# Kernel tuning notes

Measured on AMD Instinct MI355X. Metric: run time of the kernel, lower is better.

Reference implementation:

```python
import jax, jax.numpy as jnp
import numpy as np

NUM_HEADS = 16


def _rotate_half(x):
    x1, x2 = jnp.split(x, 2, axis=-1)
    return jnp.concatenate((-x2, x1), axis=-1)


def setup_inputs() -> dict:
    key = jax.random.key(0)
    ks = jax.random.split(key, 6)
    S, HID, D, W = 32768, 1280, 80, 64
    x = jax.random.normal(ks[0], (S, HID), dtype=jnp.float32)
    # rotary embeddings: use actual cos/sin of random phases for realism
    ang = jax.random.uniform(ks[1], (S, D), dtype=jnp.float32) * 6.28318
    cos = jnp.cos(ang)
    sin = jnp.sin(ang)
    # uniform windows of 64 tokens -> 512 windows
    cu_seqlens = (jnp.arange(S // W + 1, dtype=jnp.int32) * W)
    qkv_kernel = jax.random.normal(ks[2], (HID, 3 * HID), dtype=jnp.float32) * (HID ** -0.5)
    qkv_bias = jnp.zeros((3 * HID,), dtype=jnp.float32)
    proj_kernel = jax.random.normal(ks[3], (HID, HID), dtype=jnp.float32) * (HID ** -0.5)
    proj_bias = jnp.zeros((HID,), dtype=jnp.float32)
    return {"x": x, "cos": cos, "sin": sin, "cu_seqlens": cu_seqlens,
            "qkv_kernel": qkv_kernel, "qkv_bias": qkv_bias,
            "proj_kernel": proj_kernel, "proj_bias": proj_bias}


def reference(x, cos, sin, cu_seqlens, qkv_kernel, qkv_bias, proj_kernel, proj_bias):
    S, HID = x.shape
    H = NUM_HEADS
    D = HID // H
    scale = D ** -0.5

    qkv = x @ qkv_kernel + qkv_bias                      # [S, 3*HID]
    q, k, v = jnp.split(qkv, 3, axis=-1)
    q = q.reshape(S, H, D)
    k = k.reshape(S, H, D)
    v = v.reshape(S, H, D)

    c = cos[:, :D][:, None, :]                           # [S, 1, D]
    s = sin[:, :D][:, None, :]
    q = q * c + _rotate_half(q) * s
    k = k * c + _rotate_half(k) * s

    # Uniform windows: cu_seqlens = W * arange(nw+1); vectorize the per-window
    # full attention as a batched block-diagonal attention [nw, W, H, D].
    nw = cu_seqlens.shape[0] - 1
    W = S // nw
    qw = q.reshape(nw, W, H, D).astype(jnp.float32)
    kw = k.reshape(nw, W, H, D).astype(jnp.float32)
    vw = v.reshape(nw, W, H, D).astype(jnp.float32)

    scores = jnp.einsum('nqhd,nkhd->nhqk', qw, kw) * scale   # [nw, H, W, W]
    weights = jax.nn.softmax(scores, axis=-1)
    out = jnp.einsum('nhqk,nkhd->nqhd', weights, vw)          # [nw, W, H, D]
    out = out.reshape(S, HID).astype(x.dtype)
    return out @ proj_kernel + proj_bias
```

## Files before the change

kernel.cpp:

```cpp
#include <hip/hip_runtime.h>
#include <hip/hip_bf16.h>
#include <hip/hip_fp16.h>

typedef __attribute__((ext_vector_type(8))) short short8;
typedef __attribute__((ext_vector_type(4))) float f32x4;
typedef __attribute__((ext_vector_type(16))) float f32x16;
typedef unsigned short u16;
typedef unsigned int u32;

__device__ __forceinline__ u16 f2bf(float v) {
  __hip_bfloat16 h = __float2bfloat16(v);
  return __builtin_bit_cast(u16, h);
}
__device__ __forceinline__ float bf2f(u16 u) {
  return __builtin_bit_cast(float, (u32)u << 16);
}
__device__ __forceinline__ u16 f2h(float v) {
  __half h = __float2half(v);
  return __builtin_bit_cast(u16, h);
}
__device__ __forceinline__ float h2f(u16 u) {
  return __half2float(__builtin_bit_cast(__half, u));
}

__global__ __launch_bounds__(256) void casth(const float* __restrict__ X, long long n,
                                             u16* __restrict__ H) {
  long long i0 = ((long long)blockIdx.x * 256 + threadIdx.x) * 4;
  long long stride = (long long)gridDim.x * 256 * 4;
  for (long long i = i0; i < n; i += stride) {
    float4 v = *(const float4*)(X + i);
    ushort4 h;
    h.x = f2h(v.x);
    h.y = f2h(v.y);
    h.z = f2h(v.z);
    h.w = f2h(v.w);
    *(ushort4*)(H + i) = h;
  }
}

__global__ __launch_bounds__(256) void transpose_cast(const float* __restrict__ W,
    int K, int N, u16* __restrict__ T) {
  __shared__ float tile[64][65];
  const int nb = N >> 6;
  const int br = blockIdx.x / nb, bc = blockIdx.x - br * nb;
  const int tx = threadIdx.x & 63, ty = threadIdx.x >> 6;
  #pragma unroll
  for (int i = ty; i < 64; i += 4)
    tile[i][tx] = W[(size_t)(br * 64 + i) * N + bc * 64 + tx];
  __syncthreads();
  #pragma unroll
  for (int i = ty; i < 64; i += 4) {
    size_t off = (size_t)(bc * 64 + i) * K + br * 64 + tx;
    T[off] = f2h(tile[tx][i]);
  }
}

__global__ __launch_bounds__(256) void transpose_split(const float* __restrict__ W,
    int K, int N, u16* __restrict__ Thi, u16* __restrict__ Tlo) {
  __shared__ float tile[64][65];
  const int nb = N >> 6;
  const int br = blockIdx.x / nb, bc = blockIdx.x - br * nb;
  const int tx = threadIdx.x & 63, ty = threadIdx.x >> 6;
  #pragma unroll
  for (int i = ty; i < 64; i += 4)
    tile[i][tx] = W[(size_t)(br * 64 + i) * N + bc * 64 + tx];
  __syncthreads();
  #pragma unroll
  for (int i = ty; i < 64; i += 4) {
    float v = tile[tx][i];
    u16 hb = f2bf(v);
    size_t off = (size_t)(bc * 64 + i) * K + br * 64 + tx;
    Thi[off] = hb;
    Tlo[off] = f2bf(v - bf2f(hb));
  }
}

__global__ __launch_bounds__(256) void rope_qk(u16* __restrict__ qkv,
    const float* __restrict__ cosg, const float* __restrict__ sing) {
  const int idx = blockIdx.x * 256 + threadIdx.x;
  const int row = idx / 80;
  const int rem = idx - row * 80;
  const int h = rem / 5;
  const int dd = (rem - h * 5) * 8;
  u16* qp = qkv + (size_t)row * 3840 + h * 80 + dd;
  u16* kp = qp + 1280;
  const float* cp = cosg + row * 80 + dd;
  const float* sp = sing + row * 80 + dd;
  short8 qa = *(short8*)qp,        qb = *(short8*)(qp + 40);
  short8 ka = *(short8*)kp,        kb = *(short8*)(kp + 40);
  f32x4 cL0 = *(const f32x4*)cp,        cL1 = *(const f32x4*)(cp + 4);
  f32x4 sL0 = *(const f32x4*)sp,        sL1 = *(const f32x4*)(sp + 4);
  f32x4 cH0 = *(const f32x4*)(cp + 40), cH1 = *(const f32x4*)(cp + 44);
  f32x4 sH0 = *(const f32x4*)(sp + 40), sH1 = *(const f32x4*)(sp + 44);
  short8 oqa, oqb, oka, okb;
  #pragma unroll
  for (int j = 0; j < 8; ++j) {
    float cl = j < 4 ? cL0[j] : cL1[j - 4];
    float sl = j < 4 ? sL0[j] : sL1[j - 4];
    float ch = j < 4 ? cH0[j] : cH1[j - 4];
    float sh = j < 4 ? sH0[j] : sH1[j - 4];
    float qaf = h2f((u16)qa[j]), qbf = h2f((u16)qb[j]);
    float kaf = h2f((u16)ka[j]), kbf = h2f((u16)kb[j]);
    oqa[j] = (short)f2h(qaf * cl - qbf * sl);
    oqb[j] = (short)f2h(qbf * ch + qaf * sh);
    oka[j] = (short)f2h(kaf * cl - kbf * sl);
    okb[j] = (short)f2h(kbf * ch + kaf * sh);
  }
  *(short8*)qp = oqa;        *(short8*)(qp + 40) = oqb;
  *(short8*)kp = oka;        *(short8*)(kp + 40) = okb;
}

__device__ __forceinline__ void gload16(const void* g, void* l) {
  __builtin_amdgcn_global_load_lds((const __attribute__((address_space(1))) u32*)g,
                                   (__attribute__((address_space(3))) u32*)l, 16, 0, 0);
}
__device__ __forceinline__ void mfma32b(f32x16& c, short8 a, short8 b) {
  asm("v_mfma_f32_32x32x16_bf16 %0, %1, %2, %0" : "+v"(c) : "v"(a), "v"(b));
}
__device__ __forceinline__ void mfma32h(f32x16& c, short8 a, short8 b) {
  asm("v_mfma_f32_32x32x16_f16 %0, %1, %2, %0" : "+v"(c) : "v"(a), "v"(b));
}

#define CFENCE() asm volatile("" ::: "memory")
#define BAR() do { CFENCE(); __builtin_amdgcn_s_barrier(); CFENCE(); } while (0)

#define HS0 0
#define HS1 32768
#define HS2 65536

#define STAGEH(t_, sb_) do {                                                   \
  const size_t go__ = (size_t)srow * 1280 + (size_t)(t_) * 32 + skoff;         \
  char* l__ = smem + (sb_) + tid * 16;                                         \
  gload16(Ap + go__,      l__);                                                \
  gload16(Ap + go__ + 16, l__ + 8192);                                         \
  gload16(Bp + go__,      l__ + 16384);                                        \
  gload16(Bp + go__ + 16, l__ + 24576);                                        \
} while (0)

#define PHH(q_, sC_, sS_, vm4_, st_) do {                                      \
  if (vm4_) asm volatile("s_waitcnt vmcnt(4)" ::: "memory");                   \
  else      asm volatile("s_waitcnt vmcnt(0)" ::: "memory");                   \
  BAR();                                                                       \
  if (st_) STAGEH((q_) + 2, sS_);                                              \
  _Pragma("unroll")                                                            \
  for (int kk = 0; kk < 2; ++kk) {                                             \
    const char* hb__ = smem + (sC_) + kk * 8192;                               \
    short8 ah__[4], bh__[2];                                                   \
    _Pragma("unroll")                                                          \
    for (int m = 0; m < 4; ++m)                                                \
      ah__[m] = *(const short8*)(hb__ + ((wm4 + m) << 10) + laneOff);          \
    _Pragma("unroll")                                                          \
    for (int n = 0; n < 2; ++n)                                                \
      bh__[n] = *(const short8*)(hb__ + 16384 + ((wn2 + n) << 10) + laneOff);  \
    __builtin_amdgcn_s_setprio(1);                                             \
    _Pragma("unroll")                                                          \
    for (int m = 0; m < 4; ++m)                                                \
      _Pragma("unroll")                                                        \
      for (int n = 0; n < 2; ++n) mfma32h(acc[m][n], ah__[m], bh__[n]);        \
    __builtin_amdgcn_s_setprio(0);                                             \
  }                                                                            \
} while (0)

__global__ __launch_bounds__(512, 2) void gemmh(
    const u16* __restrict__ A, const u16* __restrict__ B,
    const float* __restrict__ bias, u16* __restrict__ Cout, int N) {
  __shared__ char smem[98304];
  const int tid = threadIdx.x;
  const int lane = tid & 63;
  const int l31 = lane & 31, h = lane >> 5;
  const int wave = tid >> 6;
  const int wm = wave >> 2, wn = wave & 3;
  const int wm4 = wm * 4, wn2 = wn * 2;
  const int nwg = gridDim.x;
  int tile = ((int)blockIdx.x & 7) * (nwg >> 3) + ((int)blockIdx.x >> 3);
  const int ntn = N >> 8;
  const int bm = tile / ntn, bn = tile - bm * ntn;

  const int lr = lane & 15;
  const int laneOff = ((lr >> 1) << 7) +
                      ((((((lane & 1) << 2) | (lane >> 4)) ^ (lr >> 1)) & 7) << 4);
  const int cell = tid & 63, line = cell >> 3, slotc = cell & 7;
  const int uu = slotc ^ line;
  const int lam = (uu >> 2) | (line << 1) | ((uu & 3) << 4);
  const int srow = ((tid >> 6) << 5) + (lam & 31);
  const int skoff = (lam >> 5) << 3;

  const u16* Ap = A + (size_t)bm * 256 * 1280;
  const u16* Bp = B + (size_t)bn * 256 * 1280;

  f32x16 acc[4][2];
  #pragma unroll
  for (int m = 0; m < 4; ++m)
    #pragma unroll
    for (int n = 0; n < 2; ++n)
      #pragma unroll
      for (int j = 0; j < 16; ++j) acc[m][n][j] = 0.f;

  STAGEH(0, HS0);
  STAGEH(1, HS1);

  #pragma unroll 1
  for (int g = 0; g < 12; ++g) {
    const int q = 3 * g;
    PHH(q,     HS0, HS2, 1, 1);
    PHH(q + 1, HS1, HS0, 1, 1);
    PHH(q + 2, HS2, HS1, 1, 1);
  }
  PHH(36, HS0, HS2, 1, 1);
  PHH(37, HS1, HS0, 1, 1);
  PHH(38, HS2, HS1, 1, 0);
  PHH(39, HS0, HS1, 0, 0);

  asm volatile("s_nop 7\ns_nop 7\ns_nop 7");
  #pragma unroll
  for (int n = 0; n < 2; ++n) {
    const int col = bn * 256 + wn * 64 + n * 32 + l31;
    const float bv = bias[col];
    #pragma unroll
    for (int m = 0; m < 4; ++m) {
      const int rbase = bm * 256 + wm * 128 + m * 32 + 4 * h;
      #pragma unroll
      for (int rr = 0; rr < 16; ++rr) {
        const int grow = rbase + (rr & 3) + 8 * (rr >> 2);
        Cout[(size_t)grow * N + col] = f2h(acc[m][n][rr] + bv);
      }
    }
  }
}

#define TS0 0
#define TS1 49152
#define TS2 98304

#define STAGET(t_, sb_) do {                                                   \
  const size_t go__ = (size_t)srow * 1280 + (size_t)(t_) * 32 + skoff;         \
  char* l__ = smem + (sb_) + tid * 16;                                         \
  gload16(Ah + go__,      l__);                                                \
  gload16(Ah + go__ + 16, l__ + 8192);                                         \
  gload16(Bh + go__,      l__ + 16384);                                        \
  gload16(Bh + go__ + 16, l__ + 24576);                                        \
  gload16(Bl + go__,      l__ + 32768);                                        \
  gload16(Bl + go__ + 16, l__ + 40960);                                        \
} while (0)

#define PHT(q_, sC_, sS_, vm6_, st_) do {                                      \
  if (vm6_) asm volatile("s_waitcnt vmcnt(6)" ::: "memory");                   \
  else      asm volatile("s_waitcnt vmcnt(0)" ::: "memory");                   \
  BAR();                                                                       \
  if (st_) STAGET((q_) + 2, sS_);                                              \
  _Pragma("unroll")                                                            \
  for (int kk = 0; kk < 2; ++kk) {                                             \
    const char* hb__ = smem + (sC_) + kk * 8192;                               \
    short8 ah__[4], bh__[2], bl__[2];                                          \
    _Pragma("unroll")                                                          \
    for (int m = 0; m < 4; ++m)                                                \
      ah__[m] = *(const short8*)(hb__ + ((wm4 + m) << 10) + laneOff);          \
    _Pragma("unroll")                                                          \
    for (int n = 0; n < 2; ++n) {                                              \
      bh__[n] = *(const short8*)(hb__ + 16384 + ((wn2 + n) << 10) + laneOff);  \
      bl__[n] = *(const short8*)(hb__ + 32768 + ((wn2 + n) << 10) + laneOff);  \
    }                                                                          \
    __builtin_amdgcn_s_setprio(1);                                             \
    _Pragma("unroll")                                                          \
    for (int m = 0; m < 4; ++m)                                                \
      _Pragma("unroll")                                                        \
      for (int n = 0; n < 2; ++n) mfma32b(acc[m][n], ah__[m], bh__[n]);        \
    _Pragma("unroll")                                                          \
    for (int m = 0; m < 4; ++m)                                                \
      _Pragma("unroll")                                                        \
      for (int n = 0; n < 2; ++n) mfma32b(acc[m][n], ah__[m], bl__[n]);        \
    __builtin_amdgcn_s_setprio(0);                                             \
  }                                                                            \
} while (0)

__global__ __launch_bounds__(512, 2) void gemmt(
    const u16* __restrict__ Ahi,
    const u16* __restrict__ Bhi, const u16* __restrict__ Blo,
    const float* __restrict__ bias, float* __restrict__ Cout, int N) {
  __shared__ char smem[147456];
  const int tid = threadIdx.x;
  const int lane = tid & 63;
  const int l31 = lane & 31, h = lane >> 5;
  const int wave = tid >> 6;
  const int wm = wave >> 2, wn = wave & 3;
  const int wm4 = wm * 4, wn2 = wn * 2;
  const int nwg = gridDim.x;
  int tile = ((int)blockIdx.x & 7) * (nwg >> 3) + ((int)blockIdx.x >> 3);
  const int ntn = N >> 8;
  const int bm = tile / ntn, bn = tile - bm * ntn;

  const int lr = lane & 15;
  const int laneOff = ((lr >> 1) << 7) +
                      ((((((lane & 1) << 2) | (lane >> 4)) ^ (lr >> 1)) & 7) << 4);
  const int cell = tid & 63, line = cell >> 3, slotc = cell & 7;
  const int uu = slotc ^ line;
  const int lam = (uu >> 2) | (line << 1) | ((uu & 3) << 4);
  const int srow = ((tid >> 6) << 5) + (lam & 31);
  const int skoff = (lam >> 5) << 3;

  const u16* Ah = Ahi + (size_t)bm * 256 * 1280;
  const u16* Bh = Bhi + (size_t)bn * 256 * 1280;
  const u16* Bl = Blo + (size_t)bn * 256 * 1280;

  f32x16 acc[4][2];
  #pragma unroll
  for (int m = 0; m < 4; ++m)
    #pragma unroll
    for (int n = 0; n < 2; ++n)
      #pragma unroll
      for (int j = 0; j < 16; ++j) acc[m][n][j] = 0.f;

  STAGET(0, TS0);
  STAGET(1, TS1);

  #pragma unroll 1
  for (int g = 0; g < 12; ++g) {
    const int q = 3 * g;
    PHT(q,     TS0, TS2, 1, 1);
    PHT(q + 1, TS1, TS0, 1, 1);
    PHT(q + 2, TS2, TS1, 1, 1);
  }
  PHT(36, TS0, TS2, 1, 1);
  PHT(37, TS1, TS0, 1, 1);
  PHT(38, TS2, TS1, 1, 0);
  PHT(39, TS0, TS1, 0, 0);

  asm volatile("s_nop 7\ns_nop 7\ns_nop 7");
  #pragma unroll
  for (int n = 0; n < 2; ++n) {
    const int col = bn * 256 + wn * 64 + n * 32 + l31;
    const float bv = bias[col];
    #pragma unroll
    for (int m = 0; m < 4; ++m) {
      const int rbase = bm * 256 + wm * 128 + m * 32 + 4 * h;
      #pragma unroll
      for (int rr = 0; rr < 16; ++rr) {
        const int grow = rbase + (rr & 3) + 8 * (rr >> 2);
        Cout[(size_t)grow * N + col] = acc[m][n][rr] + bv;
      }
    }
  }
}

#define ATT_SCALE 0.11180339887498949f
__global__ __launch_bounds__(256) void attn_win(const u16* __restrict__ qkv,
    u16* __restrict__ ohi) {
  __shared__ __attribute__((aligned(16))) u16 Qs[64 * 104];
  __shared__ __attribute__((aligned(16))) u16 Ks[64 * 104];
  __shared__ __attribute__((aligned(16))) u16 Vt[80 * 72];
  __shared__ __attribute__((aligned(16))) u16 Ps[64 * 72];
  const int t = threadIdx.x;
  const int w = blockIdx.x >> 4, h = blockIdx.x & 15;
  const int rowbase = w * 64;
  const int wave = t >> 6, lane = t & 63;
  const int lr = lane & 15, lg = lane >> 4;

  for (int c = t; c < 64 * 12; c += 256) {
    int s = c / 12, d8 = c - s * 12;
    short8 q8 = (short8){0,0,0,0,0,0,0,0}, k8 = (short8){0,0,0,0,0,0,0,0};
    if (d8 < 10) {
      const u16* b = qkv + (size_t)(rowbase + s) * 3840 + h * 80 + d8 * 8;
      short8 qh = *(const short8*)b;
      short8 kh = *(const short8*)(b + 1280);
      #pragma unroll
      for (int j = 0; j < 8; ++j) {
        q8[j] = (short)f2bf(h2f((u16)qh[j]));
        k8[j] = (short)f2bf(h2f((u16)kh[j]));
      }
    }
    *(short8*)&Qs[s * 104 + d8 * 8] = q8;
    *(short8*)&Ks[s * 104 + d8 * 8] = k8;
  }
  for (int c = t; c < 640; c += 256) {
    int s = c / 10, d0 = (c - s * 10) * 8;
    short8 v = *(const short8*)(qkv + (size_t)(rowbase + s) * 3840 + 2560 + h * 80 + d0);
    #pragma unroll
    for (int j = 0; j < 8; ++j) Vt[(d0 + j) * 72 + s] = f2bf(h2f((u16)v[j]));
  }
  __syncthreads();

  f32x4 sf[4];
  #pragma unroll
  for (int fc = 0; fc < 4; ++fc) sf[fc] = (f32x4){0.f, 0.f, 0.f, 0.f};
  #pragma unroll
  for (int kk = 0; kk < 3; ++kk) {
    short8 qf = *(const short8*)((const char*)Qs + (wave * 16 + lr) * 208 + kk * 64 + lg * 16);
    #pragma unroll
    for (int fc = 0; fc < 4; ++fc) {
      short8 kf = *(const short8*)((const char*)Ks + (fc * 16 + lr) * 208 + kk * 64 + lg * 16);
      asm("v_mfma_f32_16x16x32_bf16 %0, %1, %2, %0" : "+v"(sf[fc]) : "v"(qf), "v"(kf));
    }
  }
  asm volatile("s_nop 7\ns_nop 7");

  float pr[4][4];
  #pragma unroll
  for (int fc = 0; fc < 4; ++fc)
    #pragma unroll
    for (int j = 0; j < 4; ++j) pr[fc][j] = sf[fc][j] * ATT_SCALE;
  #pragma unroll
  for (int j = 0; j < 4; ++j) {
    float m = fmaxf(fmaxf(pr[0][j], pr[1][j]), fmaxf(pr[2][j], pr[3][j]));
    m = fmaxf(m, __shfl_xor(m, 1));
    m = fmaxf(m, __shfl_xor(m, 2));
    m = fmaxf(m, __shfl_xor(m, 4));
    m = fmaxf(m, __shfl_xor(m, 8));
    float sum = 0.f;
    #pragma unroll
    for (int fc = 0; fc < 4; ++fc) { pr[fc][j] = __expf(pr[fc][j] - m); sum += pr[fc][j]; }
    sum += __shfl_xor(sum, 1);
    sum += __shfl_xor(sum, 2);
    sum += __shfl_xor(sum, 4);
    sum += __shfl_xor(sum, 8);
    float inv = 1.f / sum;
    #pragma unroll
    for (int fc = 0; fc < 4; ++fc) pr[fc][j] *= inv;
  }
  #pragma unroll
  for (int j = 0; j < 4; ++j) {
    int row = wave * 16 + lg * 4 + j;
    #pragma unroll
    for (int fc = 0; fc < 4; ++fc) {
      u32 pb = (u32)f2bf(pr[fc][j]);
      u32 partner = (u32)__shfl_xor((int)pb, 1);
      if ((lr & 1) == 0)
        *(u32*)((char*)Ps + row * 144 + (fc * 16 + lr) * 2) = pb | (partner << 16);
    }
  }
  __syncthreads();

  f32x4 av[5];
  #pragma unroll
  for (int fd = 0; fd < 5; ++fd) av[fd] = (f32x4){0.f, 0.f, 0.f, 0.f};
  #pragma unroll
  for (int kk = 0; kk < 2; ++kk) {
    short8 pf = *(const short8*)((const char*)Ps + (wave * 16 + lr) * 144 + kk * 64 + lg * 16);
    #pragma unroll
    for (int fd = 0; fd < 5; ++fd) {
      short8 vf = *(const short8*)((const char*)Vt + (fd * 16 + lr) * 144 + kk * 64 + lg * 16);
      asm("v_mfma_f32_16x16x32_bf16 %0, %1, %2, %0" : "+v"(av[fd]) : "v"(pf), "v"(vf));
    }
  }
  asm volatile("s_nop 7\ns_nop 7");

  #pragma unroll
  for (int fd = 0; fd < 5; ++fd)
    #pragma unroll
    for (int j = 0; j < 4; ++j) {
      int grow = rowbase + wave * 16 + lg * 4 + j;
      size_t off = (size_t)grow * 1280 + h * 80 + fd * 16 + lr;
      ohi[off] = f2bf(av[fd][j]);
    }
}

extern "C" void kernel_launch(void* const* d_in, const int* in_sizes, int n_in,
                              void* d_out, int out_size, void* d_ws, size_t ws_size,
                              hipStream_t stream) {
  const float* x     = (const float*)d_in[0];
  const float* cosg  = (const float*)d_in[1];
  const float* sing  = (const float*)d_in[2];
  const float* wqkv  = (const float*)d_in[4];
  const float* bqkv  = (const float*)d_in[5];
  const float* wproj = (const float*)d_in[6];
  const float* bproj = (const float*)d_in[7];
  float* out = (float*)d_out;

  char* ws = (char*)d_ws;
  const size_t SZ_QKV = 251658240ull;
  const size_t SZ_X   = 83886080ull;
  const size_t SZ_WQ  = 9830400ull;
  const size_t SZ_WP  = 3276800ull;
  u16* qkv  = (u16*)(ws);
  u16* xh   = (u16*)(ws + SZ_QKV);
  u16* abf  = (u16*)(ws + SZ_QKV + SZ_X);
  u16* wqt  = (u16*)(ws + SZ_QKV + 2 * SZ_X);
  u16* wpth = (u16*)(ws + SZ_QKV + 2 * SZ_X + SZ_WQ);
  u16* wptl = (u16*)(ws + SZ_QKV + 2 * SZ_X + SZ_WQ + SZ_WP);
  if (ws_size < SZ_QKV + 2 * SZ_X + SZ_WQ + 2 * SZ_WP) return;

  casth<<<2048, 256, 0, stream>>>(x, 41943040ll, xh);
  transpose_cast<<<1200, 256, 0, stream>>>(wqkv, 1280, 3840, wqt);
  transpose_split<<<400, 256, 0, stream>>>(wproj, 1280, 1280, wpth, wptl);
  gemmh<<<1920, 512, 0, stream>>>(xh, wqt, bqkv, qkv, 3840);
  rope_qk<<<10240, 256, 0, stream>>>(qkv, cosg, sing);
  attn_win<<<8192, 256, 0, stream>>>(qkv, abf);
  gemmt<<<640, 512, 0, stream>>>(abf, wpth, wptl, bproj, out, 1280);
}
```

Baseline: 891.8 us.

## Store QKV in bf16 and drop split-precision weights in output projection

The QKV projection now writes bf16 instead of fp16, and rope and attention consume bf16 directly, which removes the fp16-to-bf16 conversions when loading into shared memory. The output projection GEMM no longer uses the hi/lo split of the weights. That halves its MFMA count and cuts shared memory per block from 144KB to 96KB. The cost is lower precision: bf16 QKV has fewer mantissa bits, and the single-bf16 proj weights drop the error-compensating term, which may hurt accuracy against the fp32 reference.

Measured after the change: 799.9 us. 1.11x faster.

```diff
diff --git a/kernel.cpp b/kernel.cpp
--- a/kernel.cpp
+++ b/kernel.cpp
@@ -75,7 +75,7 @@
   }
 }
 
-__global__ __launch_bounds__(256) void rope_qk(u16* __restrict__ qkv,
+__global__ __launch_bounds__(256) void rope_qkb(u16* __restrict__ qkv,
     const float* __restrict__ cosg, const float* __restrict__ sing) {
   const int idx = blockIdx.x * 256 + threadIdx.x;
   const int row = idx / 80;
@@ -99,12 +99,12 @@
     float sl = j < 4 ? sL0[j] : sL1[j - 4];
     float ch = j < 4 ? cH0[j] : cH1[j - 4];
     float sh = j < 4 ? sH0[j] : sH1[j - 4];
-    float qaf = h2f((u16)qa[j]), qbf = h2f((u16)qb[j]);
-    float kaf = h2f((u16)ka[j]), kbf = h2f((u16)kb[j]);
-    oqa[j] = (short)f2h(qaf * cl - qbf * sl);
-    oqb[j] = (short)f2h(qbf * ch + qaf * sh);
-    oka[j] = (short)f2h(kaf * cl - kbf * sl);
-    okb[j] = (short)f2h(kbf * ch + kaf * sh);
+    float qaf = bf2f((u16)qa[j]), qbf = bf2f((u16)qb[j]);
+    float kaf = bf2f((u16)ka[j]), kbf = bf2f((u16)kb[j]);
+    oqa[j] = (short)f2bf(qaf * cl - qbf * sl);
+    oqb[j] = (short)f2bf(qbf * ch + qaf * sh);
+    oka[j] = (short)f2bf(kaf * cl - kbf * sl);
+    okb[j] = (short)f2bf(kbf * ch + kaf * sh);
   }
   *(short8*)qp = oqa;        *(short8*)(qp + 40) = oqb;
   *(short8*)kp = oka;        *(short8*)(kp + 40) = okb;
@@ -161,7 +161,7 @@
   }                                                                            \
 } while (0)
 
-__global__ __launch_bounds__(512, 2) void gemmh(
+__global__ __launch_bounds__(512, 2) void gemmhb(
     const u16* __restrict__ A, const u16* __restrict__ B,
     const float* __restrict__ bias, u16* __restrict__ Cout, int N) {
   __shared__ char smem[98304];
@@ -222,62 +222,53 @@
       #pragma unroll
       for (int rr = 0; rr < 16; ++rr) {
         const int grow = rbase + (rr & 3) + 8 * (rr >> 2);
-        Cout[(size_t)grow * N + col] = f2h(acc[m][n][rr] + bv);
+        Cout[(size_t)grow * N + col] = f2bf(acc[m][n][rr] + bv);
       }
     }
   }
 }
 
-#define TS0 0
-#define TS1 49152
-#define TS2 98304
-
-#define STAGET(t_, sb_) do {                                                   \
+#define PS0 0
+#define PS1 32768
+#define PS2 65536
+
+#define STAGEP(t_, sb_) do {                                                   \
   const size_t go__ = (size_t)srow * 1280 + (size_t)(t_) * 32 + skoff;         \
   char* l__ = smem + (sb_) + tid * 16;                                         \
-  gload16(Ah + go__,      l__);                                                \
-  gload16(Ah + go__ + 16, l__ + 8192);                                         \
-  gload16(Bh + go__,      l__ + 16384);                                        \
-  gload16(Bh + go__ + 16, l__ + 24576);                                        \
-  gload16(Bl + go__,      l__ + 32768);                                        \
-  gload16(Bl + go__ + 16, l__ + 40960);                                        \
+  gload16(Ap + go__,      l__);                                                \
+  gload16(Ap + go__ + 16, l__ + 8192);                                         \
+  gload16(Bp + go__,      l__ + 16384);                                        \
+  gload16(Bp + go__ + 16, l__ + 24576);                                        \
 } while (0)
 
-#define PHT(q_, sC_, sS_, vm6_, st_) do {                                      \
-  if (vm6_) asm volatile("s_waitcnt vmcnt(6)" ::: "memory");                   \
+#define PHP(q_, sC_, sS_, vm4_, st_) do {                                      \
+  if (vm4_) asm volatile("s_waitcnt vmcnt(4)" ::: "memory");                   \
   else      asm volatile("s_waitcnt vmcnt(0)" ::: "memory");                   \
   BAR();                                                                       \
-  if (st_) STAGET((q_) + 2, sS_);                                              \
+  if (st_) STAGEP((q_) + 2, sS_);                                              \
   _Pragma("unroll")                                                            \
   for (int kk = 0; kk < 2; ++kk) {                                             \
     const char* hb__ = smem + (sC_) + kk * 8192;                               \
-    short8 ah__[4], bh__[2], bl__[2];                                          \
+    short8 ah__[4], bh__[2];                                                   \
     _Pragma("unroll")                                                          \
     for (int m = 0; m < 4; ++m)                                                \
       ah__[m] = *(const short8*)(hb__ + ((wm4 + m) << 10) + laneOff);          \
     _Pragma("unroll")                                                          \
-    for (int n = 0; n < 2; ++n) {                                              \
+    for (int n = 0; n < 2; ++n)                                                \
       bh__[n] = *(const short8*)(hb__ + 16384 + ((wn2 + n) << 10) + laneOff);  \
-      bl__[n] = *(const short8*)(hb__ + 32768 + ((wn2 + n) << 10) + laneOff);  \
-    }                                                                          \
     __builtin_amdgcn_s_setprio(1);                                             \
     _Pragma("unroll")                                                          \
     for (int m = 0; m < 4; ++m)                                                \
       _Pragma("unroll")                                                        \
       for (int n = 0; n < 2; ++n) mfma32b(acc[m][n], ah__[m], bh__[n]);        \
-    _Pragma("unroll")                                                          \
-    for (int m = 0; m < 4; ++m)                                                \
-      _Pragma("unroll")                                                        \
-      for (int n = 0; n < 2; ++n) mfma32b(acc[m][n], ah__[m], bl__[n]);        \
     __builtin_amdgcn_s_setprio(0);                                             \
   }                                                                            \
 } while (0)
 
-__global__ __launch_bounds__(512, 2) void gemmt(
-    const u16* __restrict__ Ahi,
-    const u16* __restrict__ Bhi, const u16* __restrict__ Blo,
+__global__ __launch_bounds__(512, 2) void gemmp1(
+    const u16* __restrict__ A, const u16* __restrict__ B,
     const float* __restrict__ bias, float* __restrict__ Cout, int N) {
-  __shared__ char smem[147456];
+  __shared__ char smem[98304];
   const int tid = threadIdx.x;
   const int lane = tid & 63;
   const int l31 = lane & 31, h = lane >> 5;
@@ -298,9 +289,8 @@
   const int srow = ((tid >> 6) << 5) + (lam & 31);
   const int skoff = (lam >> 5) << 3;
 
-  const u16* Ah = Ahi + (size_t)bm * 256 * 1280;
-  const u16* Bh = Bhi + (size_t)bn * 256 * 1280;
-  const u16* Bl = Blo + (size_t)bn * 256 * 1280;
+  const u16* Ap = A + (size_t)bm * 256 * 1280;
+  const u16* Bp = B + (size_t)bn * 256 * 1280;
 
   f32x16 acc[4][2];
   #pragma unroll
@@ -310,20 +300,20 @@
       #pragma unroll
       for (int j = 0; j < 16; ++j) acc[m][n][j] = 0.f;
 
-  STAGET(0, TS0);
-  STAGET(1, TS1);
+  STAGEP(0, PS0);
+  STAGEP(1, PS1);
 
   #pragma unroll 1
   for (int g = 0; g < 12; ++g) {
     const int q = 3 * g;
-    PHT(q,     TS0, TS2, 1, 1);
-    PHT(q + 1, TS1, TS0, 1, 1);
-    PHT(q + 2, TS2, TS1, 1, 1);
-  }
-  PHT(36, TS0, TS2, 1, 1);
-  PHT(37, TS1, TS0, 1, 1);
-  PHT(38, TS2, TS1, 1, 0);
-  PHT(39, TS0, TS1, 0, 0);
+    PHP(q,     PS0, PS2, 1, 1);
+    PHP(q + 1, PS1, PS0, 1, 1);
+    PHP(q + 2, PS2, PS1, 1, 1);
+  }
+  PHP(36, PS0, PS2, 1, 1);
+  PHP(37, PS1, PS0, 1, 1);
+  PHP(38, PS2, PS1, 1, 0);
+  PHP(39, PS0, PS1, 0, 0);
 
   asm volatile("s_nop 7\ns_nop 7\ns_nop 7");
   #pragma unroll
@@ -360,13 +350,8 @@
     short8 q8 = (short8){0,0,0,0,0,0,0,0}, k8 = (short8){0,0,0,0,0,0,0,0};
     if (d8 < 10) {
       const u16* b = qkv + (size_t)(rowbase + s) * 3840 + h * 80 + d8 * 8;
-      short8 qh = *(const short8*)b;
-      short8 kh = *(const short8*)(b + 1280);
-      #pragma unroll
-      for (int j = 0; j < 8; ++j) {
-        q8[j] = (short)f2bf(h2f((u16)qh[j]));
-        k8[j] = (short)f2bf(h2f((u16)kh[j]));
-      }
+      q8 = *(const short8*)b;
+      k8 = *(const short8*)(b + 1280);
     }
     *(short8*)&Qs[s * 104 + d8 * 8] = q8;
     *(short8*)&Ks[s * 104 + d8 * 8] = k8;
@@ -375,7 +360,7 @@
     int s = c / 10, d0 = (c - s * 10) * 8;
     short8 v = *(const short8*)(qkv + (size_t)(rowbase + s) * 3840 + 2560 + h * 80 + d0);
     #pragma unroll
-    for (int j = 0; j < 8; ++j) Vt[(d0 + j) * 72 + s] = f2bf(h2f((u16)v[j]));
+    for (int j = 0; j < 8; ++j) Vt[(d0 + j) * 72 + s] = (u16)v[j];
   }
   __syncthreads();
 
@@ -481,8 +466,8 @@
   casth<<<2048, 256, 0, stream>>>(x, 41943040ll, xh);
   transpose_cast<<<1200, 256, 0, stream>>>(wqkv, 1280, 3840, wqt);
   transpose_split<<<400, 256, 0, stream>>>(wproj, 1280, 1280, wpth, wptl);
-  gemmh<<<1920, 512, 0, stream>>>(xh, wqt, bqkv, qkv, 3840);
-  rope_qk<<<10240, 256, 0, stream>>>(qkv, cosg, sing);
+  gemmhb<<<1920, 512, 0, stream>>>(xh, wqt, bqkv, qkv, 3840);
+  rope_qkb<<<10240, 256, 0, stream>>>(qkv, cosg, sing);
   attn_win<<<8192, 256, 0, stream>>>(qkv, abf);
-  gemmt<<<640, 512, 0, stream>>>(abf, wpth, wptl, bproj, out, 1280);
-}
+  gemmp1<<<640, 512, 0, stream>>>(abf, wpth, bproj, out, 1280);
+}
```
